# Kernel tuning notes

Measured on AMD Instinct MI355X. Metric: run time of the kernel, lower is better.

The kernel has to match this reference:

```python
import jax, jax.numpy as jnp
import numpy as np

N_NODES = 50000   # gnn_nodes_num
N_EDGES = 800000  # avg degree 16
HIDDEN = 64       # hidden_channels
BATCH_Y = 2048    # |y|


def setup_inputs() -> dict:
    key = jax.random.key(0)
    ks = jax.random.split(key, 16)
    s = 0.05
    H = HIDDEN
    return {
        "x": jnp.arange(N_NODES, dtype=jnp.int32),
        "edge_index": jax.random.randint(ks[0], (2, N_EDGES), 0, N_NODES, dtype=jnp.int32),
        "y": jax.random.randint(ks[1], (BATCH_Y,), 0, N_NODES, dtype=jnp.int32),
        # learned params
        "emb": jax.random.normal(ks[2], (N_NODES, H), dtype=jnp.float32) * s,
        "Wq": jax.random.normal(ks[3], (H, H), dtype=jnp.float32) * s,
        "bq": jnp.zeros((H,), dtype=jnp.float32),
        "Wk": jax.random.normal(ks[4], (H, H), dtype=jnp.float32) * s,
        "bk": jnp.zeros((H,), dtype=jnp.float32),
        "Wv": jax.random.normal(ks[5], (H, H), dtype=jnp.float32) * s,
        "bv": jnp.zeros((H,), dtype=jnp.float32),
        "Ws": jax.random.normal(ks[6], (H, H), dtype=jnp.float32) * s,  # root/skip lin
        "bs": jnp.zeros((H,), dtype=jnp.float32),
        "W1": jax.random.normal(ks[7], (H, N_NODES), dtype=jnp.float32) * s,
        "b1": jnp.zeros((N_NODES,), dtype=jnp.float32),
    }


def reference(x, edge_index, y, emb, Wq, bq, Wk, bk, Wv, bv, Ws, bs, W1, b1):
    H = Wq.shape[1]
    h = emb[x]                                  # [N, H] embedding lookup
    src, dst = edge_index[0], edge_index[1]

    # TransformerConv (heads=1, root_weight=True): per-node projections
    q = h @ Wq + bq                             # [N, H]
    k = h @ Wk + bk
    v = h @ Wv + bv

    # attention logits per edge, softmax grouped by destination node
    logits = jnp.sum(q[dst] * k[src], axis=-1) / jnp.sqrt(jnp.float32(H))  # [E]
    m = jax.ops.segment_max(logits, dst, num_segments=N_NODES)             # [N]
    e = jnp.exp(logits - m[dst])
    denom = jax.ops.segment_sum(e, dst, num_segments=N_NODES)              # [N]
    alpha = e / denom[dst]                                                 # [E]

    agg = jax.ops.segment_sum(alpha[:, None] * v[src], dst, num_segments=N_NODES)
    out = agg + h @ Ws + bs                     # [N, H] GAT output

    # for each node u: sum of out[dst] over edges with src == u  (vectorized
    # form of the original per-y boolean-mask loop), then gather at y
    neigh = jax.ops.segment_sum(out[dst], src, num_segments=N_NODES)       # [N, H]
    new_x = neigh[y]                            # [B, H]

    return jax.nn.softmax(new_x @ W1 + b1, axis=-1)  # [B, N]
```

## Files before the change

kernel.cpp:

```cpp
#include <hip/hip_runtime.h>
#include <math.h>

#define NN 50000
#define NE 800000
#define HH 64
#define NB 2048
#define NPAD 53248
#define NST 64
#define TPS 13
#define LOG2E 1.4426950408889634f
#define HBLK 3125
#define QBLK 782

typedef __attribute__((ext_vector_type(8))) short bf16x8;
typedef __attribute__((ext_vector_type(4))) float f32x4;

__device__ inline ushort f2bf(float f) {
  uint u = __float_as_uint(f);
  uint r = (u + 0x7fffu + ((u >> 16) & 1u)) >> 16;
  return (ushort)r;
}
__device__ inline float bf2f(uint u) { return __uint_as_float(u << 16); }

__device__ inline float fexp2(float x) {
#if __has_builtin(__builtin_amdgcn_exp2f)
  return __builtin_amdgcn_exp2f(x);
#else
  return exp2f(x);
#endif
}

__global__ __launch_bounds__(256) void k_prep(
    const float* __restrict__ W1, const float* __restrict__ b1,
    const float* __restrict__ Wq, const float* __restrict__ Wk,
    const float* __restrict__ Wv, const float* __restrict__ Ws,
    ushort* __restrict__ W1T, float* __restrict__ eb, ushort* __restrict__ WT,
    int* cnt_d, int* cnt_s, char* flag, char* ymark)
{
  int i = blockIdx.x * 256 + threadIdx.x;
  if (i < NN) { cnt_d[i] = 0; cnt_s[i] = 0; flag[i] = 0; ymark[i] = 0; }
  if (i < 4 * HH * HH) {
    int m = i >> 12, rem = i & 4095;
    int c = rem >> 6, kk = rem & 63;
    const float* W = (m == 0) ? Wq : (m == 1) ? Wk : (m == 2) ? Wv : Ws;
    WT[i] = f2bf(W[kk * HH + c]);
  }
  if (i < NPAD) {
    eb[i] = (i < NN) ? __expf(b1[i]) : 0.f;
    uint4 o[8];
    ushort* op = (ushort*)o;
    if (i < NN) {
#pragma unroll
      for (int k = 0; k < HH; ++k) op[k] = f2bf(W1[(size_t)k * NN + i] * LOG2E);
    } else {
#pragma unroll
      for (int k = 0; k < HH; ++k) op[k] = 0;
    }
    uint4* dst = (uint4*)(W1T + (size_t)i * HH);
#pragma unroll
    for (int j = 0; j < 8; ++j) dst[j] = o[j];
  }
}

__global__ __launch_bounds__(256) void k_mark(const int* __restrict__ y,
                                              char* __restrict__ ymark) {
  int i = blockIdx.x * 256 + threadIdx.x;
  if (i < NB) ymark[y[i]] = 1;
}

__global__ __launch_bounds__(256) void k_hq(
    const int* __restrict__ src, const int* __restrict__ dst,
    const char* __restrict__ ymark,
    int* cnt_s, int* cnt_d, char* __restrict__ flag,
    int* __restrict__ rank_d, int* __restrict__ rank_s,
    const int* __restrict__ x, const float* __restrict__ emb,
    const ushort* __restrict__ WT,
    const float* __restrict__ bq, const float* __restrict__ bk,
    const float* __restrict__ bv, const float* __restrict__ bs,
    ushort* __restrict__ qb, ushort* __restrict__ kb, ushort* __restrict__ vb,
    float* __restrict__ hs)
{
  if (blockIdx.x < HBLK) {
    int e = blockIdx.x * 256 + threadIdx.x;
    if (e < NE) {
      int s = src[e], d = dst[e];
      rank_d[e] = atomicAdd(&cnt_d[d], 1);
      if (ymark[s]) {
        rank_s[e] = atomicAdd(&cnt_s[s], 1);
        flag[d] = 1;
      } else {
        rank_s[e] = -1;
      }
    }
    return;
  }
  int l = threadIdx.x & 63, w = threadIdx.x >> 6;
  int lr = l & 15, lk = l >> 4;
  int r0 = (blockIdx.x - HBLK) * 64;
  const ushort* wt = WT + w * HH * HH;
  const float* B = (w == 0) ? bq : (w == 1) ? bk : (w == 2) ? bv : bs;

  bf16x8 b[2][4];
#pragma unroll
  for (int kt = 0; kt < 2; ++kt)
#pragma unroll
    for (int nt = 0; nt < 4; ++nt)
      b[kt][nt] = *(const bf16x8*)(wt + (nt * 16 + lr) * HH + kt * 32 + lk * 8);

  bf16x8 a[2][4];
#pragma unroll
  for (int mt = 0; mt < 4; ++mt) {
    int row = r0 + mt * 16 + lr;
    int g = (row < NN) ? x[row] : 0;
    const float* hp = emb + (size_t)g * HH;
#pragma unroll
    for (int kt = 0; kt < 2; ++kt) {
      float4 f0 = *(const float4*)(hp + kt * 32 + lk * 8);
      float4 f1 = *(const float4*)(hp + kt * 32 + lk * 8 + 4);
      bf16x8 af;
      af[0] = f2bf(f0.x); af[1] = f2bf(f0.y); af[2] = f2bf(f0.z); af[3] = f2bf(f0.w);
      af[4] = f2bf(f1.x); af[5] = f2bf(f1.y); af[6] = f2bf(f1.z); af[7] = f2bf(f1.w);
      a[kt][mt] = af;
    }
  }

  f32x4 acc[4][4];
  const f32x4 z4 = {0.f, 0.f, 0.f, 0.f};
#pragma unroll
  for (int mt = 0; mt < 4; ++mt)
#pragma unroll
    for (int nt = 0; nt < 4; ++nt) acc[mt][nt] = z4;
#pragma unroll
  for (int kt = 0; kt < 2; ++kt)
#pragma unroll
    for (int mt = 0; mt < 4; ++mt)
#pragma unroll
      for (int nt = 0; nt < 4; ++nt)
        acc[mt][nt] = __builtin_amdgcn_mfma_f32_16x16x32_bf16(a[kt][mt], b[kt][nt], acc[mt][nt], 0, 0, 0);

  if (w < 3) {
    ushort* Db = (w == 0) ? qb : (w == 1) ? kb : vb;
#pragma unroll
    for (int mt = 0; mt < 4; ++mt)
#pragma unroll
      for (int r = 0; r < 4; ++r) {
        int row = r0 + mt * 16 + lk * 4 + r;
        if (row < NN) {
#pragma unroll
          for (int nt = 0; nt < 4; ++nt) {
            int c = nt * 16 + lr;
            Db[(size_t)row * HH + c] = f2bf(acc[mt][nt][r] + B[c]);
          }
        }
      }
  } else {
#pragma unroll
    for (int mt = 0; mt < 4; ++mt)
#pragma unroll
      for (int r = 0; r < 4; ++r) {
        int row = r0 + mt * 16 + lk * 4 + r;
        if (row < NN) {
#pragma unroll
          for (int nt = 0; nt < 4; ++nt) {
            int c = nt * 16 + lr;
            hs[(size_t)row * HH + c] = acc[mt][nt][r] + B[c];
          }
        }
      }
  }
}

__global__ __launch_bounds__(1024) void k_scan(
    const int* __restrict__ cnt_d, int* indptr_d,
    const int* __restrict__ cnt_s, int* indptr_s)
{
  const int* cnt = (blockIdx.x == 0) ? cnt_d : cnt_s;
  int* indptr    = (blockIdx.x == 0) ? indptr_d : indptr_s;
  __shared__ int sums[1024];
  const int CH = (NN + 1023) / 1024;
  int t = threadIdx.x;
  int begin = t * CH;
  int end = begin + CH; if (end > NN) end = NN;
  int s = 0;
  for (int i = begin; i < end; ++i) s += cnt[i];
  sums[t] = s;
  __syncthreads();
  for (int off = 1; off < 1024; off <<= 1) {
    int val = (t >= off) ? sums[t - off] : 0;
    __syncthreads();
    sums[t] += val;
    __syncthreads();
  }
  int prefix = (t == 0) ? 0 : sums[t - 1];
  for (int i = begin; i < end; ++i) {
    indptr[i] = prefix;
    prefix += cnt[i];
  }
  if (t == 0) indptr[NN] = sums[1023];
}

__global__ __launch_bounds__(256) void k_efill(
    const int* __restrict__ src, const int* __restrict__ dst,
    const ushort* __restrict__ qb, const ushort* __restrict__ kb,
    const char* __restrict__ flag,
    const int* __restrict__ indptr_s, const int* __restrict__ indptr_d,
    const int* __restrict__ rank_d, const int* __restrict__ rank_s,
    int* __restrict__ dstlist_s, int2* __restrict__ slot_d)
{
  int gid = blockIdx.x * 256 + threadIdx.x;
  int e = gid >> 2;
  int lane = gid & 3;
  if (e >= NE) return;
  int s = src[e], d = dst[e];
  bool fd = flag[d];
  float p = 0.f;
  if (fd) {
    const uint4* qp = (const uint4*)(qb + (size_t)d * HH + lane * 16);
    const uint4* kp = (const uint4*)(kb + (size_t)s * HH + lane * 16);
    uint4 qa0 = qp[0], ka0 = kp[0];
    uint4 qa1 = qp[1], ka1 = kp[1];
    p += bf2f(qa0.x & 0xffffu) * bf2f(ka0.x & 0xffffu) + bf2f(qa0.x >> 16) * bf2f(ka0.x >> 16);
    p += bf2f(qa0.y & 0xffffu) * bf2f(ka0.y & 0xffffu) + bf2f(qa0.y >> 16) * bf2f(ka0.y >> 16);
    p += bf2f(qa0.z & 0xffffu) * bf2f(ka0.z & 0xffffu) + bf2f(qa0.z >> 16) * bf2f(ka0.z >> 16);
    p += bf2f(qa0.w & 0xffffu) * bf2f(ka0.w & 0xffffu) + bf2f(qa0.w >> 16) * bf2f(ka0.w >> 16);
    p += bf2f(qa1.x & 0xffffu) * bf2f(ka1.x & 0xffffu) + bf2f(qa1.x >> 16) * bf2f(ka1.x >> 16);
    p += bf2f(qa1.y & 0xffffu) * bf2f(ka1.y & 0xffffu) + bf2f(qa1.y >> 16) * bf2f(ka1.y >> 16);
    p += bf2f(qa1.z & 0xffffu) * bf2f(ka1.z & 0xffffu) + bf2f(qa1.z >> 16) * bf2f(ka1.z >> 16);
    p += bf2f(qa1.w & 0xffffu) * bf2f(ka1.w & 0xffffu) + bf2f(qa1.w >> 16) * bf2f(ka1.w >> 16);
    p += __shfl_xor(p, 2);
    p += __shfl_xor(p, 1);
  }
  if (lane == 0) {
    if (fd) {
      int pd = indptr_d[d] + rank_d[e];
      int2 sl; sl.x = s; sl.y = __float_as_int(p * (0.125f * LOG2E));
      slot_d[pd] = sl;
    }
    int rs = rank_s[e];
    if (rs >= 0) dstlist_s[indptr_s[s] + rs] = d;
  }
}

__global__ __launch_bounds__(256) void k_agg(
    const int* __restrict__ indptr_d, const int2* __restrict__ slot_d,
    const ushort* __restrict__ vb, const char* __restrict__ flag,
    float* __restrict__ hs)
{
  int w = (blockIdx.x * 256 + threadIdx.x) >> 6;
  int lane = threadIdx.x & 63;
  if (w >= NN) return;
  if (!flag[w]) return;
  int beg = indptr_d[w], end = indptr_d[w + 1];
  if (beg == end) return;
  float den0 = 0.f, den1 = 0.f, acc0 = 0.f, acc1 = 0.f;
  int j = beg;
  for (; j + 1 < end; j += 2) {
    int2 sa = slot_d[j];
    int2 sb = slot_d[j + 1];
    float pa = fexp2(__int_as_float(sa.y));
    float pb = fexp2(__int_as_float(sb.y));
    float va = bf2f((uint)vb[(size_t)sa.x * HH + lane]);
    float vc = bf2f((uint)vb[(size_t)sb.x * HH + lane]);
    den0 += pa; den1 += pb;
    acc0 = fmaf(pa, va, acc0);
    acc1 = fmaf(pb, vc, acc1);
  }
  if (j < end) {
    int2 sa = slot_d[j];
    float pa = fexp2(__int_as_float(sa.y));
    den0 += pa;
    acc0 = fmaf(pa, bf2f((uint)vb[(size_t)sa.x * HH + lane]), acc0);
  }
  hs[(size_t)w * HH + lane] += (acc0 + acc1) / (den0 + den1);
}

__global__ __launch_bounds__(256) void k_newx(
    const int* __restrict__ y, const int* __restrict__ indptr_s,
    const int* __restrict__ dstlist_s, const float* __restrict__ outn,
    ushort* __restrict__ nxbf)
{
  int w = (blockIdx.x * 256 + threadIdx.x) >> 6;
  int lane = threadIdx.x & 63;
  if (w >= NB) return;
  int u = y[w];
  int beg = indptr_s[u], end = indptr_s[u + 1];
  float acc = 0.f;
  for (int j = beg; j < end; ++j) acc += outn[(size_t)dstlist_s[j] * HH + lane];
  nxbf[w * HH + lane] = f2bf(acc);
}

#define LOADA(A, t) do { int bn0_ = (t) * 64;                                    \
  _Pragma("unroll") for (int kt = 0; kt < 2; ++kt)                               \
  _Pragma("unroll") for (int nt = 0; nt < 4; ++nt)                               \
    A[kt][nt] = *(const bf16x8*)(w1t + (size_t)(bn0_ + nt * 16 + lr) * HH + kt * 32 + lk * 8); \
} while (0)

#define MFMA8(A, acc) do {                                                       \
  _Pragma("unroll") for (int kt = 0; kt < 2; ++kt)                               \
  _Pragma("unroll") for (int nt = 0; nt < 4; ++nt)                               \
    acc[nt] = __builtin_amdgcn_mfma_f32_16x16x32_bf16(A[kt][nt], bm[kt], acc[nt], 0, 0, 0); \
} while (0)

#define PROCA(A, t) do { int bn0_ = (t) * 64;                                    \
  f32x4 acc[4];                                                                  \
  _Pragma("unroll") for (int nt = 0; nt < 4; ++nt) acc[nt] = z4;                 \
  MFMA8(A, acc);                                                                 \
  _Pragma("unroll") for (int nt = 0; nt < 4; ++nt) {                             \
    int n0 = bn0_ + nt * 16 + lk * 4;                                            \
    f32x4 e4 = *(const f32x4*)(eb + n0);                                         \
    _Pragma("unroll") for (int r = 0; r < 4; ++r)                                \
      se += fexp2(acc[nt][r]) * e4[r];                                           \
  }                                                                              \
} while (0)

#define PROCB(A, t) do { int bn0_ = (t) * 64;                                    \
  f32x4 acc[4];                                                                  \
  _Pragma("unroll") for (int nt = 0; nt < 4; ++nt) acc[nt] = z4;                 \
  MFMA8(A, acc);                                                                 \
  _Pragma("unroll") for (int nt = 0; nt < 4; ++nt) {                             \
    int n0 = bn0_ + nt * 16 + lk * 4;                                            \
    f32x4 e4 = *(const f32x4*)(eb + n0);                                         \
    f32x4 vx;                                                                    \
    _Pragma("unroll") for (int r = 0; r < 4; ++r)                                \
      vx[r] = fexp2(acc[nt][r]) * e4[r] * sv;                                    \
    if (n0 < NN)                                                                 \
      __builtin_nontemporal_store(vx, (f32x4*)(out + (size_t)(r0 + lr) * NN + n0)); \
  }                                                                              \
} while (0)

__global__ __launch_bounds__(256, 4) void k_finA(
    const ushort* __restrict__ nxbf, const ushort* __restrict__ w1t,
    const float* __restrict__ eb, float* __restrict__ Spart)
{
  int tid = threadIdx.x;
  int l = tid & 63, w = tid >> 6;
  int lr = l & 15, lk = l >> 4;
  int b = blockIdx.x;
  int st = (b & 7) * 8 + ((b >> 3) & 7);
  int r0 = ((b >> 6) * 4 + w) * 16;
  int tile0 = st * TPS;
  const f32x4 z4 = {0.f, 0.f, 0.f, 0.f};

  bf16x8 bm[2];
#pragma unroll
  for (int kt = 0; kt < 2; ++kt)
    bm[kt] = *(const bf16x8*)(nxbf + (size_t)(r0 + lr) * HH + kt * 32 + lk * 8);

  float se = 0.f;
  {
    bf16x8 A0[2][4], A1[2][4];
    LOADA(A0, tile0);
#pragma unroll
    for (int i = 0; i < 6; ++i) {
      LOADA(A1, tile0 + 2 * i + 1);
      PROCA(A0, tile0 + 2 * i);
      LOADA(A0, tile0 + 2 * i + 2);
      PROCA(A1, tile0 + 2 * i + 1);
    }
    PROCA(A0, tile0 + 12);
  }
  se += __shfl_xor(se, 16);
  se += __shfl_xor(se, 32);
  if (lk == 0) Spart[(r0 + lr) * NST + st] = se;
}

__global__ __launch_bounds__(256) void k_sinv(const float* __restrict__ Spart,
                                              float* __restrict__ Sinv) {
  int r = blockIdx.x * 256 + threadIdx.x;
  if (r < NB) {
    float s = 0.f;
#pragma unroll
    for (int j = 0; j < NST; ++j) s += Spart[r * NST + j];
    Sinv[r] = 1.0f / s;
  }
}

__global__ __launch_bounds__(256, 4) void k_finB(
    const ushort* __restrict__ nxbf, const ushort* __restrict__ w1t,
    const float* __restrict__ eb, const float* __restrict__ Sinv,
    float* __restrict__ out)
{
  int tid = threadIdx.x;
  int l = tid & 63, w = tid >> 6;
  int lr = l & 15, lk = l >> 4;
  int b = blockIdx.x;
  int st = (b & 7) * 8 + ((b >> 3) & 7);
  int r0 = ((b >> 6) * 4 + w) * 16;
  int tile0 = st * TPS;
  const f32x4 z4 = {0.f, 0.f, 0.f, 0.f};

  bf16x8 bm[2];
#pragma unroll
  for (int kt = 0; kt < 2; ++kt)
    bm[kt] = *(const bf16x8*)(nxbf + (size_t)(r0 + lr) * HH + kt * 32 + lk * 8);

  float sv = Sinv[r0 + lr];

  {
    bf16x8 A0[2][4], A1[2][4];
    LOADA(A0, tile0);
#pragma unroll
    for (int i = 0; i < 6; ++i) {
      LOADA(A1, tile0 + 2 * i + 1);
      PROCB(A0, tile0 + 2 * i);
      LOADA(A0, tile0 + 2 * i + 2);
      PROCB(A1, tile0 + 2 * i + 1);
    }
    PROCB(A0, tile0 + 12);
  }
}

extern "C" void kernel_launch(void* const* d_in, const int* in_sizes, int n_in,
                              void* d_out, int out_size, void* d_ws, size_t ws_size,
                              hipStream_t stream)
{
  const int* x   = (const int*)d_in[0];
  const int* src = (const int*)d_in[1];
  const int* dst = src + NE;
  const int* y   = (const int*)d_in[2];
  const float* emb = (const float*)d_in[3];
  const float* Wq = (const float*)d_in[4];  const float* bq = (const float*)d_in[5];
  const float* Wk = (const float*)d_in[6];  const float* bk = (const float*)d_in[7];
  const float* Wv = (const float*)d_in[8];  const float* bv = (const float*)d_in[9];
  const float* Ws = (const float*)d_in[10]; const float* bs = (const float*)d_in[11];
  const float* W1 = (const float*)d_in[12]; const float* b1 = (const float*)d_in[13];
  float* out = (float*)d_out;

  char* wsb = (char*)d_ws;
  ushort* nxbf  = (ushort*)wsb;
  ushort* w1t   = (ushort*)(wsb + 262144);
  float*  Spart = (float*)(wsb + 7077888);
  float*  Sinv  = (float*)(wsb + 7602176);
  float*  eb    = (float*)(wsb + 7610368);
  const size_t PERS  = 7823360;
  const size_t BIGSZ = 46400000;
  char* big = (ws_size >= PERS + BIGSZ) ? (wsb + PERS) : (char*)d_out;
  ushort* qb     = (ushort*)(big + 0);
  ushort* kb     = (ushort*)(big + 6400000);
  ushort* vb     = (ushort*)(big + 12800000);
  float*  hs     = (float*)(big + 19200000);
  int2*   slot_d = (int2*)(big + 32000000);
  int* dstlist_s = (int*)(big + 38400000);
  int* rank_d    = (int*)(big + 38700000);
  int* rank_s    = (int*)(big + 41900000);
  int* cnt_d     = (int*)(big + 45100000);
  int* cnt_s     = (int*)(big + 45300000);
  int* indptr_d  = (int*)(big + 45500000);
  int* indptr_s  = (int*)(big + 45700064);
  char* flag     = (char*)(big + 45900128);
  char* ymark    = (char*)(big + 45950176);
  ushort* WT     = (ushort*)(big + 46000224);

  k_prep<<<dim3(224), dim3(256), 0, stream>>>(W1, b1, Wq, Wk, Wv, Ws, w1t, eb, WT,
                                              cnt_d, cnt_s, flag, ymark);
  k_mark<<<dim3(8), dim3(256), 0, stream>>>(y, ymark);
  k_hq<<<dim3(HBLK + QBLK), dim3(256), 0, stream>>>(src, dst, ymark,
                                                    cnt_s, cnt_d, flag, rank_d, rank_s,
                                                    x, emb, WT, bq, bk, bv, bs,
                                                    qb, kb, vb, hs);
  k_scan<<<dim3(2), dim3(1024), 0, stream>>>(cnt_d, indptr_d, cnt_s, indptr_s);
  k_efill<<<dim3(12500), dim3(256), 0, stream>>>(src, dst, qb, kb, flag,
                                                 indptr_s, indptr_d, rank_d, rank_s,
                                                 dstlist_s, slot_d);
  k_agg<<<dim3(12500), dim3(256), 0, stream>>>(indptr_d, slot_d, vb, flag, hs);
  k_newx<<<dim3(512), dim3(256), 0, stream>>>(y, indptr_s, dstlist_s, hs, nxbf);
  k_finA<<<dim3(2048), dim3(256), 0, stream>>>(nxbf, w1t, eb, Spart);
  k_sinv<<<dim3(8), dim3(256), 0, stream>>>(Spart, Sinv);
  k_finB<<<dim3(2048), dim3(256), 0, stream>>>(nxbf, w1t, eb, Sinv, out);
}
```

Baseline: 465.9 us.

## Fuse softmax passes into one persistent kernel with grid barrier and pre-tiled W1

Merges the row-sum pass, the reciprocal kernel and the output pass into one kernel of 256 blocks of 1024 threads. The blocks meet at an atomic grid-wide barrier, and each lane then sums its row's partials directly. W1 is pre-packed into the MFMA fragment layout so each tile loads contiguously. The explicit double-buffered loads become a plain loop. This removes two launches and the Sinv round trip. It risks deadlock if the 256 blocks are not all resident at once, and the simpler loop may hide less load latency.

Result: slower. 490.8 us (+5.3%).

```diff
diff --git a/kernel.cpp b/kernel.cpp
--- a/kernel.cpp
+++ b/kernel.cpp
@@ -6,8 +6,8 @@
 #define HH 64
 #define NB 2048
 #define NPAD 53248
-#define NST 64
-#define TPS 13
+#define NST2 32
+#define TPS2 26
 #define LOG2E 1.4426950408889634f
 #define HBLK 3125
 #define QBLK 782
@@ -34,11 +34,12 @@
     const float* __restrict__ W1, const float* __restrict__ b1,
     const float* __restrict__ Wq, const float* __restrict__ Wk,
     const float* __restrict__ Wv, const float* __restrict__ Ws,
-    ushort* __restrict__ W1T, float* __restrict__ eb, ushort* __restrict__ WT,
-    int* cnt_d, int* cnt_s, char* flag, char* ymark)
+    ushort* __restrict__ w1p, float* __restrict__ eb, ushort* __restrict__ WT,
+    int* cnt_d, int* cnt_s, char* flag, char* ymark, int* bar)
 {
   int i = blockIdx.x * 256 + threadIdx.x;
   if (i < NN) { cnt_d[i] = 0; cnt_s[i] = 0; flag[i] = 0; ymark[i] = 0; }
+  if (i == 0) *bar = 0;
   if (i < 4 * HH * HH) {
     int m = i >> 12, rem = i & 4095;
     int c = rem >> 6, kk = rem & 63;
@@ -56,9 +57,13 @@
 #pragma unroll
       for (int k = 0; k < HH; ++k) op[k] = 0;
     }
-    uint4* dst = (uint4*)(W1T + (size_t)i * HH);
-#pragma unroll
-    for (int j = 0; j < 8; ++j) dst[j] = o[j];
+    int t = i >> 6, nt = (i >> 4) & 3, lr = i & 15;
+    ushort* tp = w1p + (size_t)t * 4096;
+#pragma unroll
+    for (int kt = 0; kt < 2; ++kt)
+#pragma unroll
+      for (int lk = 0; lk < 4; ++lk)
+        *(uint4*)(tp + (kt * 4 + nt) * 512 + (lk * 16 + lr) * 8) = o[kt * 4 + lk];
   }
 }
 
@@ -289,10 +294,10 @@
   nxbf[w * HH + lane] = f2bf(acc);
 }
 
-#define LOADA(A, t) do { int bn0_ = (t) * 64;                                    \
+#define LOADP(A, t) do { const ushort* tp_ = w1p + (size_t)(t) * 4096;           \
   _Pragma("unroll") for (int kt = 0; kt < 2; ++kt)                               \
   _Pragma("unroll") for (int nt = 0; nt < 4; ++nt)                               \
-    A[kt][nt] = *(const bf16x8*)(w1t + (size_t)(bn0_ + nt * 16 + lr) * HH + kt * 32 + lk * 8); \
+    A[kt][nt] = *(const bf16x8*)(tp_ + (kt * 4 + nt) * 512 + l * 8);             \
 } while (0)
 
 #define MFMA8(A, acc) do {                                                       \
@@ -328,17 +333,18 @@
   }                                                                              \
 } while (0)
 
-__global__ __launch_bounds__(256, 4) void k_finA(
-    const ushort* __restrict__ nxbf, const ushort* __restrict__ w1t,
-    const float* __restrict__ eb, float* __restrict__ Spart)
+__global__ __launch_bounds__(1024, 4) void k_fin(
+    const ushort* __restrict__ nxbf, const ushort* __restrict__ w1p,
+    const float* __restrict__ eb, float* __restrict__ Spart,
+    int* __restrict__ bar, float* __restrict__ out)
 {
   int tid = threadIdx.x;
   int l = tid & 63, w = tid >> 6;
   int lr = l & 15, lk = l >> 4;
   int b = blockIdx.x;
-  int st = (b & 7) * 8 + ((b >> 3) & 7);
-  int r0 = ((b >> 6) * 4 + w) * 16;
-  int tile0 = st * TPS;
+  int st = b & 31;
+  int r0 = ((b >> 5) * 16 + w) * 16;
+  int tile0 = st * TPS2;
   const f32x4 z4 = {0.f, 0.f, 0.f, 0.f};
 
   bf16x8 bm[2];
@@ -348,65 +354,44 @@
 
   float se = 0.f;
   {
-    bf16x8 A0[2][4], A1[2][4];
-    LOADA(A0, tile0);
-#pragma unroll
-    for (int i = 0; i < 6; ++i) {
-      LOADA(A1, tile0 + 2 * i + 1);
-      PROCA(A0, tile0 + 2 * i);
-      LOADA(A0, tile0 + 2 * i + 2);
-      PROCA(A1, tile0 + 2 * i + 1);
-    }
-    PROCA(A0, tile0 + 12);
+    bf16x8 A0[2][4];
+#pragma unroll 2
+    for (int t = 0; t < TPS2; ++t) {
+      LOADP(A0, tile0 + t);
+      PROCA(A0, tile0 + t);
+    }
   }
   se += __shfl_xor(se, 16);
   se += __shfl_xor(se, 32);
-  if (lk == 0) Spart[(r0 + lr) * NST + st] = se;
-}
-
-__global__ __launch_bounds__(256) void k_sinv(const float* __restrict__ Spart,
-                                              float* __restrict__ Sinv) {
-  int r = blockIdx.x * 256 + threadIdx.x;
-  if (r < NB) {
-    float s = 0.f;
-#pragma unroll
-    for (int j = 0; j < NST; ++j) s += Spart[r * NST + j];
-    Sinv[r] = 1.0f / s;
-  }
-}
-
-__global__ __launch_bounds__(256, 4) void k_finB(
-    const ushort* __restrict__ nxbf, const ushort* __restrict__ w1t,
-    const float* __restrict__ eb, const float* __restrict__ Sinv,
-    float* __restrict__ out)
-{
-  int tid = threadIdx.x;
-  int l = tid & 63, w = tid >> 6;
-  int lr = l & 15, lk = l >> 4;
-  int b = blockIdx.x;
-  int st = (b & 7) * 8 + ((b >> 3) & 7);
-  int r0 = ((b >> 6) * 4 + w) * 16;
-  int tile0 = st * TPS;
-  const f32x4 z4 = {0.f, 0.f, 0.f, 0.f};
-
-  bf16x8 bm[2];
-#pragma unroll
-  for (int kt = 0; kt < 2; ++kt)
-    bm[kt] = *(const bf16x8*)(nxbf + (size_t)(r0 + lr) * HH + kt * 32 + lk * 8);
-
-  float sv = Sinv[r0 + lr];
-
+  if (lk == 0)
+    __hip_atomic_store(&Spart[(r0 + lr) * NST2 + st], se,
+                       __ATOMIC_RELAXED, __HIP_MEMORY_SCOPE_AGENT);
+
+  __threadfence();
+  __syncthreads();
+  if (tid == 0) {
+    __hip_atomic_fetch_add(bar, 1, __ATOMIC_ACQ_REL, __HIP_MEMORY_SCOPE_AGENT);
+    while (__hip_atomic_load(bar, __ATOMIC_ACQUIRE, __HIP_MEMORY_SCOPE_AGENT) < 256)
+      __builtin_amdgcn_s_sleep(2);
+  }
+  __syncthreads();
+
+  float s = 0.f;
   {
-    bf16x8 A0[2][4], A1[2][4];
-    LOADA(A0, tile0);
-#pragma unroll
-    for (int i = 0; i < 6; ++i) {
-      LOADA(A1, tile0 + 2 * i + 1);
-      PROCB(A0, tile0 + 2 * i);
-      LOADA(A0, tile0 + 2 * i + 2);
-      PROCB(A1, tile0 + 2 * i + 1);
-    }
-    PROCB(A0, tile0 + 12);
+    int myrow = r0 + lr;
+    for (int j = 0; j < NST2; ++j)
+      s += __hip_atomic_load(&Spart[myrow * NST2 + j],
+                             __ATOMIC_RELAXED, __HIP_MEMORY_SCOPE_AGENT);
+  }
+  float sv = 1.0f / s;
+
+  {
+    bf16x8 A0[2][4];
+#pragma unroll 2
+    for (int t = 0; t < TPS2; ++t) {
+      LOADP(A0, tile0 + t);
+      PROCB(A0, tile0 + t);
+    }
   }
 }
 
@@ -428,11 +413,11 @@
 
   char* wsb = (char*)d_ws;
   ushort* nxbf  = (ushort*)wsb;
-  ushort* w1t   = (ushort*)(wsb + 262144);
+  ushort* w1p   = (ushort*)(wsb + 262144);
   float*  Spart = (float*)(wsb + 7077888);
-  float*  Sinv  = (float*)(wsb + 7602176);
-  float*  eb    = (float*)(wsb + 7610368);
-  const size_t PERS  = 7823360;
+  int*    bar   = (int*)(wsb + 7340032);
+  float*  eb    = (float*)(wsb + 7340160);
+  const size_t PERS  = 7553152;
   const size_t BIGSZ = 46400000;
   char* big = (ws_size >= PERS + BIGSZ) ? (wsb + PERS) : (char*)d_out;
   ushort* qb     = (ushort*)(big + 0);
@@ -451,8 +436,8 @@
   char* ymark    = (char*)(big + 45950176);
   ushort* WT     = (ushort*)(big + 46000224);
 
-  k_prep<<<dim3(224), dim3(256), 0, stream>>>(W1, b1, Wq, Wk, Wv, Ws, w1t, eb, WT,
-                                              cnt_d, cnt_s, flag, ymark);
+  k_prep<<<dim3(224), dim3(256), 0, stream>>>(W1, b1, Wq, Wk, Wv, Ws, w1p, eb, WT,
+                                              cnt_d, cnt_s, flag, ymark, bar);
   k_mark<<<dim3(8), dim3(256), 0, stream>>>(y, ymark);
   k_hq<<<dim3(HBLK + QBLK), dim3(256), 0, stream>>>(src, dst, ymark,
                                                     cnt_s, cnt_d, flag, rank_d, rank_s,
@@ -464,7 +449,5 @@
                                                  dstlist_s, slot_d);
   k_agg<<<dim3(12500), dim3(256), 0, stream>>>(indptr_d, slot_d, vb, flag, hs);
   k_newx<<<dim3(512), dim3(256), 0, stream>>>(y, indptr_s, dstlist_s, hs, nxbf);
-  k_finA<<<dim3(2048), dim3(256), 0, stream>>>(nxbf, w1t, eb, Spart);
-  k_sinv<<<dim3(8), dim3(256), 0, stream>>>(Spart, Sinv);
-  k_finB<<<dim3(2048), dim3(256), 0, stream>>>(nxbf, w1t, eb, Sinv, out);
-}
+  k_fin<<<dim3(256), dim3(1024), 0, stream>>>(nxbf, w1p, eb, Spart, bar, out);
+}
```

## Store unnormalized fp16 softmax numerators, then normalize in a streaming pass

Applied to the files above, without the earlier changes.

When the workspace is large enough, the final softmax now runs the W1 matmul and exp once. Each unnormalized numerator is written as fp16 to a scratch buffer through a swizzled LDS transpose, and a second streaming kernel scales it into the fp32 output. This replaces the old recompute of matmul plus exp in a second pass. W1^T is also prepacked into an MFMA-fragment layout so tile loads are contiguous, and the stat tiling changes to 52 strips of 16 tiles. The cost is an extra ~200MB of fp16 write and read plus reduced fp16 precision, and the fallback path loses its software double-buffering.

Measured after the change: 439.9 us (median of 2 runs). 1.06x faster.

```diff
diff --git a/kernel.cpp b/kernel.cpp
--- a/kernel.cpp
+++ b/kernel.cpp
@@ -6,8 +6,8 @@
 #define HH 64
 #define NB 2048
 #define NPAD 53248
-#define NST 64
-#define TPS 13
+#define NST3 52
+#define TPS3 16
 #define LOG2E 1.4426950408889634f
 #define HBLK 3125
 #define QBLK 782
@@ -34,7 +34,7 @@
     const float* __restrict__ W1, const float* __restrict__ b1,
     const float* __restrict__ Wq, const float* __restrict__ Wk,
     const float* __restrict__ Wv, const float* __restrict__ Ws,
-    ushort* __restrict__ W1T, float* __restrict__ eb, ushort* __restrict__ WT,
+    ushort* __restrict__ w1p, float* __restrict__ eb, ushort* __restrict__ WT,
     int* cnt_d, int* cnt_s, char* flag, char* ymark)
 {
   int i = blockIdx.x * 256 + threadIdx.x;
@@ -56,9 +56,13 @@
 #pragma unroll
       for (int k = 0; k < HH; ++k) op[k] = 0;
     }
-    uint4* dst = (uint4*)(W1T + (size_t)i * HH);
-#pragma unroll
-    for (int j = 0; j < 8; ++j) dst[j] = o[j];
+    int t = i >> 6, nt = (i >> 4) & 3, lr = i & 15;
+    ushort* tp = w1p + (size_t)t * 4096;
+#pragma unroll
+    for (int kt = 0; kt < 2; ++kt)
+#pragma unroll
+      for (int lk = 0; lk < 4; ++lk)
+        *(uint4*)(tp + (kt * 4 + nt) * 512 + (lk * 16 + lr) * 8) = o[kt * 4 + lk];
   }
 }
 
@@ -289,10 +293,10 @@
   nxbf[w * HH + lane] = f2bf(acc);
 }
 
-#define LOADA(A, t) do { int bn0_ = (t) * 64;                                    \
+#define LOADP(A, t) do { const ushort* tp_ = w1p + (size_t)(t) * 4096;           \
   _Pragma("unroll") for (int kt = 0; kt < 2; ++kt)                               \
   _Pragma("unroll") for (int nt = 0; nt < 4; ++nt)                               \
-    A[kt][nt] = *(const bf16x8*)(w1t + (size_t)(bn0_ + nt * 16 + lr) * HH + kt * 32 + lk * 8); \
+    A[kt][nt] = *(const bf16x8*)(tp_ + (kt * 4 + nt) * 512 + l * 8);             \
 } while (0)
 
 #define MFMA8(A, acc) do {                                                       \
@@ -300,6 +304,99 @@
   _Pragma("unroll") for (int nt = 0; nt < 4; ++nt)                               \
     acc[nt] = __builtin_amdgcn_mfma_f32_16x16x32_bf16(A[kt][nt], bm[kt], acc[nt], 0, 0, 0); \
 } while (0)
+
+__global__ __launch_bounds__(256) void k_finZ(
+    const ushort* __restrict__ nxbf, const ushort* __restrict__ w1p,
+    const float* __restrict__ eb, ushort* __restrict__ zb,
+    float* __restrict__ Spart)
+{
+  __shared__ ushort lt[4][16][512];
+  int tid = threadIdx.x;
+  int l = tid & 63, w = tid >> 6;
+  int lr = l & 15, lk = l >> 4;
+  int b = blockIdx.x;
+  int st = b % NST3, rg = b / NST3;
+  int r0 = rg * 64 + w * 16;
+  int tile0 = st * TPS3;
+  const f32x4 z4 = {0.f, 0.f, 0.f, 0.f};
+
+  bf16x8 bm[2];
+#pragma unroll
+  for (int kt = 0; kt < 2; ++kt)
+    bm[kt] = *(const bf16x8*)(nxbf + (size_t)(r0 + lr) * HH + kt * 32 + lk * 8);
+
+  float se = 0.f;
+#pragma unroll
+  for (int s = 0; s < 2; ++s) {
+#pragma unroll
+    for (int t = 0; t < 8; ++t) {
+      int tile = tile0 + s * 8 + t;
+      bf16x8 A0[2][4];
+      LOADP(A0, tile);
+      f32x4 acc[4];
+#pragma unroll
+      for (int nt = 0; nt < 4; ++nt) acc[nt] = z4;
+      MFMA8(A0, acc);
+#pragma unroll
+      for (int nt = 0; nt < 4; ++nt) {
+        int n0 = tile * 64 + nt * 16 + lk * 4;
+        f32x4 e4 = *(const f32x4*)(eb + n0);
+        union { _Float16 h[4]; uint2 u; } pk;
+#pragma unroll
+        for (int r = 0; r < 4; ++r) {
+          float ur = fexp2(acc[nt][r]) * e4[r];
+          se += ur;
+          pk.h[r] = (_Float16)ur;
+        }
+        int uL = t * 16 + nt * 4 + lk;
+        int uP = uL ^ (2 * (lr & 7));
+        *(uint2*)&lt[w][lr][uP * 4] = pk.u;
+      }
+    }
+    int colbase = (tile0 + s * 8) * 64;
+#pragma unroll
+    for (int r = 0; r < 16; ++r) {
+      uint4 v = *(const uint4*)&lt[w][r][(l ^ (r & 7)) * 8];
+      *(uint4*)(zb + (size_t)(r0 + r) * NPAD + colbase + l * 8) = v;
+    }
+  }
+  se += __shfl_xor(se, 16);
+  se += __shfl_xor(se, 32);
+  if (lk == 0) Spart[(r0 + lr) * NST3 + st] = se;
+}
+
+__global__ __launch_bounds__(256) void k_sinv(const float* __restrict__ Spart,
+                                              float* __restrict__ Sinv) {
+  int r = blockIdx.x * 256 + threadIdx.x;
+  if (r < NB) {
+    float s = 0.f;
+#pragma unroll
+    for (int j = 0; j < NST3; ++j) s += Spart[r * NST3 + j];
+    Sinv[r] = 1.0f / s;
+  }
+}
+
+__global__ __launch_bounds__(256) void k_finN(
+    const ushort* __restrict__ zb, const float* __restrict__ Sinv,
+    float* __restrict__ out)
+{
+  int r = blockIdx.x;
+  float sv = Sinv[r];
+  const ushort* zr = zb + (size_t)r * NPAD;
+  float* orow = out + (size_t)r * NN;
+  for (int c0 = threadIdx.x * 8; c0 < NN; c0 += 2048) {
+    uint4 zv = *(const uint4*)(zr + c0);
+    const _Float16* hp = (const _Float16*)&zv;
+    f32x4 v0, v1;
+#pragma unroll
+    for (int j = 0; j < 4; ++j) {
+      v0[j] = (float)hp[j] * sv;
+      v1[j] = (float)hp[4 + j] * sv;
+    }
+    *(f32x4*)(orow + c0) = v0;
+    *(f32x4*)(orow + c0 + 4) = v1;
+  }
+}
 
 #define PROCA(A, t) do { int bn0_ = (t) * 64;                                    \
   f32x4 acc[4];                                                                  \
@@ -329,54 +426,34 @@
 } while (0)
 
 __global__ __launch_bounds__(256, 4) void k_finA(
-    const ushort* __restrict__ nxbf, const ushort* __restrict__ w1t,
+    const ushort* __restrict__ nxbf, const ushort* __restrict__ w1p,
     const float* __restrict__ eb, float* __restrict__ Spart)
 {
   int tid = threadIdx.x;
   int l = tid & 63, w = tid >> 6;
   int lr = l & 15, lk = l >> 4;
   int b = blockIdx.x;
-  int st = (b & 7) * 8 + ((b >> 3) & 7);
-  int r0 = ((b >> 6) * 4 + w) * 16;
-  int tile0 = st * TPS;
+  int st = b % NST3, rg = b / NST3;
+  int r0 = rg * 64 + w * 16;
+  int tile0 = st * TPS3;
   const f32x4 z4 = {0.f, 0.f, 0.f, 0.f};
-
   bf16x8 bm[2];
 #pragma unroll
   for (int kt = 0; kt < 2; ++kt)
     bm[kt] = *(const bf16x8*)(nxbf + (size_t)(r0 + lr) * HH + kt * 32 + lk * 8);
-
   float se = 0.f;
   {
-    bf16x8 A0[2][4], A1[2][4];
-    LOADA(A0, tile0);
-#pragma unroll
-    for (int i = 0; i < 6; ++i) {
-      LOADA(A1, tile0 + 2 * i + 1);
-      PROCA(A0, tile0 + 2 * i);
-      LOADA(A0, tile0 + 2 * i + 2);
-      PROCA(A1, tile0 + 2 * i + 1);
-    }
-    PROCA(A0, tile0 + 12);
+    bf16x8 A0[2][4];
+#pragma unroll
+    for (int t = 0; t < TPS3; ++t) { LOADP(A0, tile0 + t); PROCA(A0, tile0 + t); }
   }
   se += __shfl_xor(se, 16);
   se += __shfl_xor(se, 32);
-  if (lk == 0) Spart[(r0 + lr) * NST + st] = se;
-}
-
-__global__ __launch_bounds__(256) void k_sinv(const float* __restrict__ Spart,
-                                              float* __restrict__ Sinv) {
-  int r = blockIdx.x * 256 + threadIdx.x;
-  if (r < NB) {
-    float s = 0.f;
-#pragma unroll
-    for (int j = 0; j < NST; ++j) s += Spart[r * NST + j];
-    Sinv[r] = 1.0f / s;
-  }
+  if (lk == 0) Spart[(r0 + lr) * NST3 + st] = se;
 }
 
 __global__ __launch_bounds__(256, 4) void k_finB(
-    const ushort* __restrict__ nxbf, const ushort* __restrict__ w1t,
+    const ushort* __restrict__ nxbf, const ushort* __restrict__ w1p,
     const float* __restrict__ eb, const float* __restrict__ Sinv,
     float* __restrict__ out)
 {
@@ -384,29 +461,19 @@
   int l = tid & 63, w = tid >> 6;
   int lr = l & 15, lk = l >> 4;
   int b = blockIdx.x;
-  int st = (b & 7) * 8 + ((b >> 3) & 7);
-  int r0 = ((b >> 6) * 4 + w) * 16;
-  int tile0 = st * TPS;
+  int st = b % NST3, rg = b / NST3;
+  int r0 = rg * 64 + w * 16;
+  int tile0 = st * TPS3;
   const f32x4 z4 = {0.f, 0.f, 0.f, 0.f};
-
   bf16x8 bm[2];
 #pragma unroll
   for (int kt = 0; kt < 2; ++kt)
     bm[kt] = *(const bf16x8*)(nxbf + (size_t)(r0 + lr) * HH + kt * 32 + lk * 8);
-
   float sv = Sinv[r0 + lr];
-
   {
-    bf16x8 A0[2][4], A1[2][4];
-    LOADA(A0, tile0);
-#pragma unroll
-    for (int i = 0; i < 6; ++i) {
-      LOADA(A1, tile0 + 2 * i + 1);
-      PROCB(A0, tile0 + 2 * i);
-      LOADA(A0, tile0 + 2 * i + 2);
-      PROCB(A1, tile0 + 2 * i + 1);
-    }
-    PROCB(A0, tile0 + 12);
+    bf16x8 A0[2][4];
+#pragma unroll
+    for (int t = 0; t < TPS3; ++t) { LOADP(A0, tile0 + t); PROCB(A0, tile0 + t); }
   }
 }
 
@@ -428,13 +495,18 @@
 
   char* wsb = (char*)d_ws;
   ushort* nxbf  = (ushort*)wsb;
-  ushort* w1t   = (ushort*)(wsb + 262144);
+  ushort* w1p   = (ushort*)(wsb + 262144);
   float*  Spart = (float*)(wsb + 7077888);
-  float*  Sinv  = (float*)(wsb + 7602176);
-  float*  eb    = (float*)(wsb + 7610368);
-  const size_t PERS  = 7823360;
-  const size_t BIGSZ = 46400000;
-  char* big = (ws_size >= PERS + BIGSZ) ? (wsb + PERS) : (char*)d_out;
+  float*  Sinv  = (float*)(wsb + 7503872);
+  float*  eb    = (float*)(wsb + 7512064);
+  const size_t PERS   = 7725056;
+  const size_t ZSZ    = (size_t)NB * NPAD * 2;
+  const size_t PERS_Z = PERS + ZSZ;
+  const size_t BIGSZ  = 46400000;
+  bool zpath = ws_size >= PERS_Z + BIGSZ;
+  ushort* zb = (ushort*)(wsb + PERS);
+  char* big = zpath ? (wsb + PERS_Z)
+                    : ((ws_size >= PERS + BIGSZ) ? (wsb + PERS) : (char*)d_out);
   ushort* qb     = (ushort*)(big + 0);
   ushort* kb     = (ushort*)(big + 6400000);
   ushort* vb     = (ushort*)(big + 12800000);
@@ -451,7 +523,7 @@
   char* ymark    = (char*)(big + 45950176);
   ushort* WT     = (ushort*)(big + 46000224);
 
-  k_prep<<<dim3(224), dim3(256), 0, stream>>>(W1, b1, Wq, Wk, Wv, Ws, w1t, eb, WT,
+  k_prep<<<dim3(224), dim3(256), 0, stream>>>(W1, b1, Wq, Wk, Wv, Ws, w1p, eb, WT,
                                               cnt_d, cnt_s, flag, ymark);
   k_mark<<<dim3(8), dim3(256), 0, stream>>>(y, ymark);
   k_hq<<<dim3(HBLK + QBLK), dim3(256), 0, stream>>>(src, dst, ymark,
@@ -464,7 +536,13 @@
                                                  dstlist_s, slot_d);
   k_agg<<<dim3(12500), dim3(256), 0, stream>>>(indptr_d, slot_d, vb, flag, hs);
   k_newx<<<dim3(512), dim3(256), 0, stream>>>(y, indptr_s, dstlist_s, hs, nxbf);
-  k_finA<<<dim3(2048), dim3(256), 0, stream>>>(nxbf, w1t, eb, Spart);
-  k_sinv<<<dim3(8), dim3(256), 0, stream>>>(Spart, Sinv);
-  k_finB<<<dim3(2048), dim3(256), 0, stream>>>(nxbf, w1t, eb, Sinv, out);
-}
+  if (zpath) {
+    k_finZ<<<dim3(NST3 * 32), dim3(256), 0, stream>>>(nxbf, w1p, eb, zb, Spart);
+    k_sinv<<<dim3(8), dim3(256), 0, stream>>>(Spart, Sinv);
+    k_finN<<<dim3(NB), dim3(256), 0, stream>>>(zb, Sinv, out);
+  } else {
+    k_finA<<<dim3(NST3 * 32), dim3(256), 0, stream>>>(nxbf, w1p, eb, Spart);
+    k_sinv<<<dim3(8), dim3(256), 0, stream>>>(Spart, Sinv);
+    k_finB<<<dim3(NST3 * 32), dim3(256), 0, stream>>>(nxbf, w1p, eb, Sinv, out);
+  }
+}
```
